# Performance work log

Measured on AMD Instinct MI355X. Metric: run time of the kernel, lower is better.

Reference implementation:

```python
import jax, jax.numpy as jnp
import numpy as np

N_NODES = 1_000_000
D = 128
B = 1024
S1 = 25   # layer-1 (inner) fanout, FLAGS.samples_1
S2 = 10   # layer-2 (outer) fanout, FLAGS.samples_2


def setup_inputs() -> dict:
    key = jax.random.key(0)
    ks = jax.random.split(key, 8)
    features = jax.random.normal(ks[0], (N_NODES, D), dtype=jnp.float32)
    scale = 1.0 / np.sqrt(D)
    W_self_0 = jax.random.normal(ks[1], (D, D), dtype=jnp.float32) * scale
    W_neigh_0 = jax.random.normal(ks[2], (D, D), dtype=jnp.float32) * scale
    W_self_1 = jax.random.normal(ks[3], (D, D), dtype=jnp.float32) * scale
    W_neigh_1 = jax.random.normal(ks[4], (D, D), dtype=jnp.float32) * scale
    samples0 = jax.random.randint(ks[5], (B,), 0, N_NODES, dtype=jnp.int32)
    samples1 = jax.random.randint(ks[6], (B * S2,), 0, N_NODES, dtype=jnp.int32)
    samples2 = jax.random.randint(ks[7], (B * S2 * S1,), 0, N_NODES, dtype=jnp.int32)
    return {
        "features": features,
        "W_self_0": W_self_0, "W_neigh_0": W_neigh_0,
        "W_self_1": W_self_1, "W_neigh_1": W_neigh_1,
        "samples0": samples0, "samples1": samples1, "samples2": samples2,
    }


def _mean_agg(self_vecs, neigh_vecs, W_self, W_neigh, act):
    # MeanAggregator: mean over neighbor axis, two dense transforms, add (concat=False)
    neigh_means = jnp.mean(neigh_vecs, axis=1)  # [n, d]
    out = self_vecs @ W_self + neigh_means @ W_neigh
    return act(out)


def reference(features, W_self_0, W_neigh_0, W_self_1, W_neigh_1,
              samples0, samples1, samples2):
    # embedding gathers for each hop (the irregular-access hot path)
    h0 = features[samples0]    # [B, D]
    h1 = features[samples1]    # [B*S2, D]
    h2 = features[samples2]    # [B*S2*S1, D]

    # layer 0 (relu): aggregate hop1->hop0 and hop2->hop1
    nh0 = _mean_agg(h0, h1.reshape(B, S2, D), W_self_0, W_neigh_0, jax.nn.relu)
    nh1 = _mean_agg(h1, h2.reshape(B * S2, S1, D), W_self_0, W_neigh_0, jax.nn.relu)

    # layer 1 (final, identity act): aggregate hop1->hop0
    out = _mean_agg(nh0, nh1.reshape(B, S2, D), W_self_1, W_neigh_1, lambda x: x)
    return out  # [B, D]
```

## Files before the change

### kernel.cpp

```cpp
#include <hip/hip_runtime.h>

typedef float f4 __attribute__((ext_vector_type(4)));

constexpr int D  = 128;
constexpr int B  = 1024;
constexpr int S1 = 25;
constexpr int S2 = 10;

constexpr int RPB = 16;

template <int NB>
__device__ __forceinline__ void gather_phase(
    const float* __restrict__ feat, const int* __restrict__ self_idx,
    const int* __restrict__ neigh_idx, int base,
    float (*lds_h)[D], float (*lds_m)[D])
{
    const int t  = threadIdx.x;
    const int l  = t & 31;
    const int rg = t >> 5;
    const int rA = rg;
    const int rB = rg + 8;

    const int* __restrict__ idxA = neigh_idx + (long)(base + rA) * NB;
    const int* __restrict__ idxB = neigh_idx + (long)(base + rB) * NB;

    f4 acc0 = {0.f, 0.f, 0.f, 0.f};
    f4 acc1 = {0.f, 0.f, 0.f, 0.f};
    #pragma unroll
    for (int s = 0; s < NB; ++s) {
        acc0 += *((const f4*)(feat + (long)idxA[s] * D) + l);
        acc1 += *((const f4*)(feat + (long)idxB[s] * D) + l);
    }
    const f4 selfA = *((const f4*)(feat + (long)self_idx[base + rA] * D) + l);
    const f4 selfB = *((const f4*)(feat + (long)self_idx[base + rB] * D) + l);

    constexpr float inv = 1.f / NB;
    *(f4*)(&lds_m[rA][l * 4]) = acc0 * inv;
    *(f4*)(&lds_m[rB][l * 4]) = acc1 * inv;
    *(f4*)(&lds_h[rA][l * 4]) = selfA;
    *(f4*)(&lds_h[rB][l * 4]) = selfB;
}

__global__ __launch_bounds__(256, 3) void layer0_fused_kernel(
    const float* __restrict__ feat,
    const int* __restrict__ s0, const int* __restrict__ s1,
    const int* __restrict__ s2,
    const float* __restrict__ Ws0, const float* __restrict__ Wn0,
    float* __restrict__ nh1, float* __restrict__ nh0)
{
    __shared__ float lds_h[RPB][D];
    __shared__ float lds_m[RPB][D];
    const int NB1 = (B * S2) / RPB;
    const int b = blockIdx.x;

    float* out;
    int base;
    if (b < NB1) {
        base = b * RPB;
        gather_phase<S1>(feat, s1, s2, base, lds_h, lds_m);
        out = nh1;
    } else {
        base = (b - NB1) * RPB;
        gather_phase<S2>(feat, s0, s1, base, lds_h, lds_m);
        out = nh0;
    }
    __syncthreads();

    const int tid = threadIdx.x;
    const int d   = tid & 127;
    const int rh  = tid >> 7;

    float acc[RPB / 2];
    #pragma unroll
    for (int r = 0; r < RPB / 2; ++r) acc[r] = 0.f;

    #pragma unroll 4
    for (int k4 = 0; k4 < D / 4; ++k4) {
        const int k = k4 * 4;
        const float ws0 = Ws0[(k + 0) * D + d];
        const float ws1 = Ws0[(k + 1) * D + d];
        const float ws2 = Ws0[(k + 2) * D + d];
        const float ws3 = Ws0[(k + 3) * D + d];
        const float wn0 = Wn0[(k + 0) * D + d];
        const float wn1 = Wn0[(k + 1) * D + d];
        const float wn2 = Wn0[(k + 2) * D + d];
        const float wn3 = Wn0[(k + 3) * D + d];
        #pragma unroll
        for (int r = 0; r < RPB / 2; ++r) {
            const int rr = rh * (RPB / 2) + r;
            const f4 hv = *(const f4*)(&lds_h[rr][k]);
            const f4 mv = *(const f4*)(&lds_m[rr][k]);
            acc[r] += hv.x * ws0 + hv.y * ws1 + hv.z * ws2 + hv.w * ws3
                    + mv.x * wn0 + mv.y * wn1 + mv.z * wn2 + mv.w * wn3;
        }
    }

    #pragma unroll
    for (int r = 0; r < RPB / 2; ++r)
        out[(long)(base + rh * (RPB / 2) + r) * D + d] = fmaxf(acc[r], 0.f);
}

constexpr int RPB_L = 4;
__global__ __launch_bounds__(128) void layer1_kernel(
    const float* __restrict__ nh0, const float* __restrict__ nh1,
    const float* __restrict__ Ws1, const float* __restrict__ Wn1,
    float* __restrict__ out)
{
    __shared__ float lds_h[RPB_L][D];
    __shared__ float lds_m[RPB_L][D];
    const int tid  = threadIdx.x;
    const int base = blockIdx.x * RPB_L;

    #pragma unroll
    for (int r = 0; r < RPB_L; ++r) {
        const int row = base + r;
        lds_h[r][tid] = nh0[(long)row * D + tid];
        float s = 0.f;
        #pragma unroll
        for (int n = 0; n < S2; ++n)
            s += nh1[((long)row * S2 + n) * D + tid];
        lds_m[r][tid] = s * (1.f / S2);
    }
    __syncthreads();

    const int d = tid;
    float acc[RPB_L];
    #pragma unroll
    for (int r = 0; r < RPB_L; ++r) acc[r] = 0.f;

    #pragma unroll 4
    for (int k4 = 0; k4 < D / 4; ++k4) {
        const int k = k4 * 4;
        const float ws0 = Ws1[(k + 0) * D + d];
        const float ws1 = Ws1[(k + 1) * D + d];
        const float ws2 = Ws1[(k + 2) * D + d];
        const float ws3 = Ws1[(k + 3) * D + d];
        const float wn0 = Wn1[(k + 0) * D + d];
        const float wn1 = Wn1[(k + 1) * D + d];
        const float wn2 = Wn1[(k + 2) * D + d];
        const float wn3 = Wn1[(k + 3) * D + d];
        #pragma unroll
        for (int r = 0; r < RPB_L; ++r) {
            const f4 hv = *(const f4*)(&lds_h[r][k]);
            const f4 mv = *(const f4*)(&lds_m[r][k]);
            acc[r] += hv.x * ws0 + hv.y * ws1 + hv.z * ws2 + hv.w * ws3
                    + mv.x * wn0 + mv.y * wn1 + mv.z * wn2 + mv.w * wn3;
        }
    }

    #pragma unroll
    for (int r = 0; r < RPB_L; ++r)
        out[(long)(base + r) * D + d] = acc[r];
}

extern "C" void kernel_launch(void* const* d_in, const int* in_sizes, int n_in,
                              void* d_out, int out_size, void* d_ws, size_t ws_size,
                              hipStream_t stream)
{
    const float* feat = (const float*)d_in[0];
    const float* Ws0  = (const float*)d_in[1];
    const float* Wn0  = (const float*)d_in[2];
    const float* Ws1  = (const float*)d_in[3];
    const float* Wn1  = (const float*)d_in[4];
    const int*   s0   = (const int*)d_in[5];
    const int*   s1   = (const int*)d_in[6];
    const int*   s2   = (const int*)d_in[7];
    float* out = (float*)d_out;

    float* nh1 = (float*)d_ws;
    float* nh0 = nh1 + (size_t)(B * S2) * D;

    const int grid0 = (B * S2) / RPB + B / RPB;
    layer0_fused_kernel<<<grid0, 256, 0, stream>>>(feat, s0, s1, s2, Ws0, Wn0, nh1, nh0);
    layer1_kernel<<<B / RPB_L, 128, 0, stream>>>(nh0, nh1, Ws1, Wn1, out);
}
```

Measured before the change: 55.21 us.

## Warp-specialize layer0 into persistent producer/consumer pipeline with double-buffered LDS

Layer 0 becomes a persistent kernel with 256 blocks. Each block loops over 2-3 tiles. Half the threads gather the next tile's features into a double-buffered LDS slot while the other half run the dense transform on the current tile, so gather latency overlaps with compute. In exchange, only half the threads issue gathers, the unroll-1 row loop leaves fewer loads in flight per thread, and the grid is much smaller, which may leave the memory system underutilized.

```diff
diff --git a/kernel.cpp b/kernel.cpp
--- a/kernel.cpp
+++ b/kernel.cpp
@@ -7,97 +7,100 @@
 constexpr int S1 = 25;
 constexpr int S2 = 10;
 
-constexpr int RPB = 16;
+constexpr int TR    = 16;
+constexpr int NT1   = (B * S2) / TR;
+constexpr int NT    = NT1 + B / TR;
+constexpr int GRID0 = 256;
 
 template <int NB>
-__device__ __forceinline__ void gather_phase(
+__device__ __forceinline__ void gather_tile(
     const float* __restrict__ feat, const int* __restrict__ self_idx,
-    const int* __restrict__ neigh_idx, int base,
+    const int* __restrict__ neigh_idx, int base, int t,
     float (*lds_h)[D], float (*lds_m)[D])
 {
-    const int t  = threadIdx.x;
     const int l  = t & 31;
     const int rg = t >> 5;
-    const int rA = rg;
-    const int rB = rg + 8;
-
-    const int* __restrict__ idxA = neigh_idx + (long)(base + rA) * NB;
-    const int* __restrict__ idxB = neigh_idx + (long)(base + rB) * NB;
-
-    f4 acc0 = {0.f, 0.f, 0.f, 0.f};
-    f4 acc1 = {0.f, 0.f, 0.f, 0.f};
-    #pragma unroll
-    for (int s = 0; s < NB; ++s) {
-        acc0 += *((const f4*)(feat + (long)idxA[s] * D) + l);
-        acc1 += *((const f4*)(feat + (long)idxB[s] * D) + l);
+    #pragma unroll 1
+    for (int rr = 0; rr < 4; ++rr) {
+        const int r = rg + rr * 4;
+        const int* __restrict__ idx = neigh_idx + (long)(base + r) * NB;
+        f4 acc = {0.f, 0.f, 0.f, 0.f};
+        #pragma unroll
+        for (int s = 0; s < NB; ++s)
+            acc += *((const f4*)(feat + (long)idx[s] * D) + l);
+        const f4 sv = *((const f4*)(feat + (long)self_idx[base + r] * D) + l);
+        *(f4*)(&lds_m[r][l * 4]) = acc * (1.f / NB);
+        *(f4*)(&lds_h[r][l * 4]) = sv;
     }
-    const f4 selfA = *((const f4*)(feat + (long)self_idx[base + rA] * D) + l);
-    const f4 selfB = *((const f4*)(feat + (long)self_idx[base + rB] * D) + l);
-
-    constexpr float inv = 1.f / NB;
-    *(f4*)(&lds_m[rA][l * 4]) = acc0 * inv;
-    *(f4*)(&lds_m[rB][l * 4]) = acc1 * inv;
-    *(f4*)(&lds_h[rA][l * 4]) = selfA;
-    *(f4*)(&lds_h[rB][l * 4]) = selfB;
 }
 
-__global__ __launch_bounds__(256, 3) void layer0_fused_kernel(
+__global__ __launch_bounds__(256, 3) void layer0_pipe_kernel(
     const float* __restrict__ feat,
     const int* __restrict__ s0, const int* __restrict__ s1,
     const int* __restrict__ s2,
     const float* __restrict__ Ws0, const float* __restrict__ Wn0,
     float* __restrict__ nh1, float* __restrict__ nh0)
 {
-    __shared__ float lds_h[RPB][D];
-    __shared__ float lds_m[RPB][D];
-    const int NB1 = (B * S2) / RPB;
+    __shared__ float lds_h[2][TR][D];
+    __shared__ float lds_m[2][TR][D];
+
     const int b = blockIdx.x;
+    const int t = threadIdx.x;
+    const int ntl = (b + 2 * GRID0 < NT) ? 3 : 2;
 
-    float* out;
-    int base;
-    if (b < NB1) {
-        base = b * RPB;
-        gather_phase<S1>(feat, s1, s2, base, lds_h, lds_m);
-        out = nh1;
-    } else {
-        base = (b - NB1) * RPB;
-        gather_phase<S2>(feat, s0, s1, base, lds_h, lds_m);
-        out = nh0;
+    if (t < 128) {
+        if (b < NT1) gather_tile<S1>(feat, s1, s2, b * TR, t, lds_h[0], lds_m[0]);
+        else         gather_tile<S2>(feat, s0, s1, (b - NT1) * TR, t, lds_h[0], lds_m[0]);
     }
     __syncthreads();
 
-    const int tid = threadIdx.x;
-    const int d   = tid & 127;
-    const int rh  = tid >> 7;
+    for (int i = 0; i < ntl; ++i) {
+        if (t < 128) {
+            if (i + 1 < ntl) {
+                const int tt = b + (i + 1) * GRID0;
+                const int bf = (i + 1) & 1;
+                if (tt < NT1)
+                    gather_tile<S1>(feat, s1, s2, tt * TR, t, lds_h[bf], lds_m[bf]);
+                else
+                    gather_tile<S2>(feat, s0, s1, (tt - NT1) * TR, t, lds_h[bf], lds_m[bf]);
+            }
+        } else {
+            const int tt   = b + i * GRID0;
+            float* __restrict__ out = (tt < NT1) ? nh1 : nh0;
+            const int base = (tt < NT1) ? tt * TR : (tt - NT1) * TR;
+            const int d    = t - 128;
+            const int bf   = i & 1;
 
-    float acc[RPB / 2];
-    #pragma unroll
-    for (int r = 0; r < RPB / 2; ++r) acc[r] = 0.f;
+            float acc[TR];
+            #pragma unroll
+            for (int r = 0; r < TR; ++r) acc[r] = 0.f;
 
-    #pragma unroll 4
-    for (int k4 = 0; k4 < D / 4; ++k4) {
-        const int k = k4 * 4;
-        const float ws0 = Ws0[(k + 0) * D + d];
-        const float ws1 = Ws0[(k + 1) * D + d];
-        const float ws2 = Ws0[(k + 2) * D + d];
-        const float ws3 = Ws0[(k + 3) * D + d];
-        const float wn0 = Wn0[(k + 0) * D + d];
-        const float wn1 = Wn0[(k + 1) * D + d];
-        const float wn2 = Wn0[(k + 2) * D + d];
-        const float wn3 = Wn0[(k + 3) * D + d];
-        #pragma unroll
-        for (int r = 0; r < RPB / 2; ++r) {
-            const int rr = rh * (RPB / 2) + r;
-            const f4 hv = *(const f4*)(&lds_h[rr][k]);
-            const f4 mv = *(const f4*)(&lds_m[rr][k]);
-            acc[r] += hv.x * ws0 + hv.y * ws1 + hv.z * ws2 + hv.w * ws3
-                    + mv.x * wn0 + mv.y * wn1 + mv.z * wn2 + mv.w * wn3;
+            #pragma unroll 4
+            for (int k4 = 0; k4 < D / 4; ++k4) {
+                const int k = k4 * 4;
+                const float ws0 = Ws0[(k + 0) * D + d];
+                const float ws1 = Ws0[(k + 1) * D + d];
+                const float ws2 = Ws0[(k + 2) * D + d];
+                const float ws3 = Ws0[(k + 3) * D + d];
+                const float wn0 = Wn0[(k + 0) * D + d];
+                const float wn1 = Wn0[(k + 1) * D + d];
+                const float wn2 = Wn0[(k + 2) * D + d];
+                const float wn3 = Wn0[(k + 3) * D + d];
+                #pragma unroll
+                for (int r = 0; r < TR; ++r) {
+                    const f4 hv = *(const f4*)(&lds_h[bf][r][k]);
+                    const f4 mv = *(const f4*)(&lds_m[bf][r][k]);
+                    acc[r] += hv.x * ws0 + hv.y * ws1 + hv.z * ws2 + hv.w * ws3
+                            + mv.x * wn0 + mv.y * wn1 + mv.z * wn2 + mv.w * wn3;
+                }
+            }
+
+            #pragma unroll
+            for (int r = 0; r < TR; ++r)
+                out[(long)(base + r) * D + d] = fmaxf(acc[r], 0.f);
         }
+        __syncthreads();
     }
-
-    #pragma unroll
-    for (int r = 0; r < RPB / 2; ++r)
-        out[(long)(base + rh * (RPB / 2) + r) * D + d] = fmaxf(acc[r], 0.f);
 }
 
 constexpr int RPB_L = 4;
@@ -170,7 +173,6 @@
     float* nh1 = (float*)d_ws;
     float* nh0 = nh1 + (size_t)(B * S2) * D;
 
-    const int grid0 = (B * S2) / RPB + B / RPB;
-    layer0_fused_kernel<<<grid0, 256, 0, stream>>>(feat, s0, s1, s2, Ws0, Wn0, nh1, nh0);
+    layer0_pipe_kernel<<<GRID0, 256, 0, stream>>>(feat, s0, s1, s2, Ws0, Wn0, nh1, nh0);
     layer1_kernel<<<B / RPB_L, 128, 0, stream>>>(nh0, nh1, Ws1, Wn1, out);
 }
```

Result: slower. 99.99 us (+81.1%).
